# Kernel tuning notes

Hardware: AMD Instinct MI355X
Metric: run time of the kernel (lower is better)

The kernel has to match this reference:

```python
import jax, jax.numpy as jnp
import numpy as np

D_MODEL = 2048
N_HEADS = 16
HEAD_DIM = D_MODEL // N_HEADS
B, T = 4, 2048


def setup_inputs() -> dict:
    key = jax.random.key(0)
    ks = jax.random.split(key, 10)
    s = 1.0 / np.sqrt(D_MODEL)
    x = jax.random.normal(ks[0], (B, T, D_MODEL), dtype=jnp.float32)
    # causal additive mask, broadcastable to [B, H, T, T]
    neg = jnp.finfo(jnp.float32).min
    causal = jnp.triu(jnp.full((T, T), neg, dtype=jnp.float32), k=1)
    mask = causal[None, None, :, :]
    return {
        "x": x,
        "mask": mask,
        "Wq": jax.random.uniform(ks[1], (D_MODEL, D_MODEL), jnp.float32, -s, s),
        "bq": jax.random.uniform(ks[2], (D_MODEL,), jnp.float32, -s, s),
        "Wk": jax.random.uniform(ks[3], (D_MODEL, HEAD_DIM), jnp.float32, -s, s),
        "bk": jax.random.uniform(ks[4], (HEAD_DIM,), jnp.float32, -s, s),
        "Wv": jax.random.uniform(ks[5], (D_MODEL, HEAD_DIM), jnp.float32, -s, s),
        "bv": jax.random.uniform(ks[6], (HEAD_DIM,), jnp.float32, -s, s),
        "Wo": jax.random.uniform(ks[7], (D_MODEL, D_MODEL), jnp.float32, -s, s),
        "bo": jax.random.uniform(ks[8], (D_MODEL,), jnp.float32, -s, s),
    }


def reference(x, mask, Wq, bq, Wk, bk, Wv, bv, Wo, bo):
    Bb, Tt, _ = x.shape
    H, Dh = N_HEADS, HEAD_DIM
    scale = 1.0 / jnp.sqrt(jnp.float32(Dh))
    q = (x @ Wq + bq).reshape(Bb, Tt, H, Dh)          # [B,T,H,D]
    k = x @ Wk + bk                                    # [B,T,D] (single KV head)
    v = x @ Wv + bv                                    # [B,T,D]
    # scores: [B,H,T,T] — q heads against shared k
    attn = jnp.einsum("bthd,bsd->bhts", q, k) * scale
    attn = attn + mask
    attn = jax.nn.softmax(attn, axis=-1)
    out = jnp.einsum("bhts,bsd->bthd", attn, v).reshape(Bb, Tt, D_MODEL)
    return out @ Wo + bo
```

## Files before the change

kernel.cpp:

```cpp
#include <hip/hip_runtime.h>
#include <hip/hip_bf16.h>
#include <stdint.h>

#define DEV __device__ __forceinline__

typedef unsigned short u16;
typedef unsigned int u32;
typedef __bf16 bf16x8 __attribute__((ext_vector_type(8)));
typedef float f32x4 __attribute__((ext_vector_type(4)));
typedef u16 u16x4 __attribute__((ext_vector_type(4)));
typedef u32 u32x4 __attribute__((ext_vector_type(4)));

typedef __attribute__((address_space(1))) u32 u32_as1;
typedef __attribute__((address_space(3))) u32 u32_as3;

static constexpr int Bn = 4, Tn = 2048, Dm = 2048, Hn = 16, Dh = 128;
static constexpr int BT = Bn * Tn;
static constexpr int KVSTR = 256;
static constexpr float CL2 = 0.1275174147f;

#define VMCNT(n) asm volatile("s_waitcnt vmcnt(" #n ")" ::: "memory")
#define BARRIER() __builtin_amdgcn_s_barrier()

DEV u16 f2bf(float f) {
  u32 u = __builtin_bit_cast(u32, f);
  u += 0x7fffu + ((u >> 16) & 1u);
  return (u16)(u >> 16);
}
DEV u16 cvt_bf(float f) { return __builtin_bit_cast(u16, (__bf16)f); }
DEV u32 cvt_pk_bf16(float lo, float hi) {
  u32 r;
  asm("v_cvt_pk_bf16_f32 %0, %1, %2" : "=v"(r) : "v"(lo), "v"(hi));
  return r;
}
DEV float max3f(float a, float b, float c) {
  float d;
  asm("v_max3_f32 %0, %1, %2, %3" : "=v"(d) : "v"(a), "v"(b), "v"(c));
  return d;
}

DEV void gl2lds16(const void* g, void* l) {
  __builtin_amdgcn_global_load_lds((u32_as1*)(uintptr_t)g,
                                   (u32_as3*)(u32)(uintptr_t)l, 16, 0, 0);
}

__global__ __launch_bounds__(256) void k_cast_bf16(const float* __restrict__ in,
                                                   u16* __restrict__ out, int n4) {
  int i = blockIdx.x * 256 + threadIdx.x;
  int stride = gridDim.x * 256;
  for (; i < n4; i += stride) {
    f32x4 v = ((const f32x4*)in)[i];
    u16x4 o;
    o.x = f2bf(v.x); o.y = f2bf(v.y); o.z = f2bf(v.z); o.w = f2bf(v.w);
    ((u16x4*)out)[i] = o;
  }
}

__global__ __launch_bounds__(256) void k_transpose_cast(const float* __restrict__ in,
                                                        u16* __restrict__ out,
                                                        int R, int C) {
  __shared__ float t[32][33];
  const int r0 = blockIdx.y * 32, c0 = blockIdx.x * 32;
  const int x = threadIdx.x, y = threadIdx.y;
#pragma unroll
  for (int i = 0; i < 4; ++i)
    t[y + i * 8][x] = in[(size_t)(r0 + y + i * 8) * C + c0 + x];
  __syncthreads();
#pragma unroll
  for (int i = 0; i < 4; ++i)
    out[(size_t)(c0 + y + i * 8) * R + r0 + x] = f2bf(t[x][y + i * 8]);
}

__global__ __launch_bounds__(256) void k_transpose_v(const u16* __restrict__ in,
                                                     int inStride,
                                                     u16* __restrict__ out,
                                                     int R, int C) {
  __shared__ u16 t[32][34];
  const int r0 = blockIdx.y * 32, c0 = blockIdx.x * 32;
  const int x = threadIdx.x, y = threadIdx.y;
#pragma unroll
  for (int i = 0; i < 4; ++i)
    t[y + i * 8][x] = in[(size_t)(r0 + y + i * 8) * inStride + c0 + x];
  __syncthreads();
  const int sx = (((x & 7) >> 2) << 4) | (((x >> 3) & 3) << 2) | (x & 3);
#pragma unroll
  for (int i = 0; i < 4; ++i)
    out[(size_t)(c0 + y + i * 8) * R + r0 + x] = t[sx][y + i * 8];
}

__global__ void k_concat_bias(const float* __restrict__ a, const float* __restrict__ b,
                              float* __restrict__ dst) {
  int i = threadIdx.x;
  dst[i] = (i < 128) ? a[i] : b[i - 128];
}

template <typename OutT>
__global__ __launch_bounds__(256) void k_gemm_bt(const u16* __restrict__ A,
                                                 const u16* __restrict__ Bt,
                                                 const float* __restrict__ bias,
                                                 OutT* __restrict__ C,
                                                 int M, int N, int K) {
  __shared__ __align__(128) char smem[32768];
  char* As = smem;
  char* Bs = smem + 16384;
  const int tid = threadIdx.x;
  const int wid = tid >> 6, lane = tid & 63;
  const int g = lane >> 4, r = lane & 15;
  const int wr = wid >> 1, wc = wid & 1;
  const int m0 = blockIdx.x * 128, n0 = blockIdx.y * 128;

  f32x4 acc[4][4];
#pragma unroll
  for (int m = 0; m < 4; ++m)
#pragma unroll
    for (int n = 0; n < 4; ++n) acc[m][n] = (f32x4)(0.f);

  for (int k0 = 0; k0 < K; k0 += 64) {
#pragma unroll
    for (int n = 0; n < 4; ++n) {
      const int L = n * 4096 + tid * 16;
      const int row = L >> 7;
      const int colb = (L & 127) ^ ((row & 7) << 4);
      gl2lds16((const char*)A + ((size_t)(m0 + row) * K + k0) * 2 + colb, As + L);
      gl2lds16((const char*)Bt + ((size_t)(n0 + row) * K + k0) * 2 + colb, Bs + L);
    }
    __syncthreads();
#pragma unroll
    for (int kk = 0; kk < 2; ++kk) {
      bf16x8 a[4], b[4];
#pragma unroll
      for (int m = 0; m < 4; ++m) {
        const int row = wr * 64 + m * 16 + r;
        a[m] = *(const bf16x8*)(As + row * 128 + ((kk * 64 + g * 16) ^ ((row & 7) << 4)));
      }
#pragma unroll
      for (int n = 0; n < 4; ++n) {
        const int row = wc * 64 + n * 16 + r;
        b[n] = *(const bf16x8*)(Bs + row * 128 + ((kk * 64 + g * 16) ^ ((row & 7) << 4)));
      }
#pragma unroll
      for (int m = 0; m < 4; ++m)
#pragma unroll
        for (int n = 0; n < 4; ++n)
          acc[m][n] = __builtin_amdgcn_mfma_f32_16x16x32_bf16(a[m], b[n], acc[m][n], 0, 0, 0);
    }
    __syncthreads();
  }

#pragma unroll
  for (int n = 0; n < 4; ++n) {
    const int col = n0 + wc * 64 + n * 16 + r;
    const float bv = bias[col];
#pragma unroll
    for (int m = 0; m < 4; ++m) {
#pragma unroll
      for (int j = 0; j < 4; ++j) {
        const int grow = m0 + wr * 64 + m * 16 + 4 * g + j;
        const float v = acc[m][n][j] + bv;
        if constexpr (sizeof(OutT) == 2)
          ((u16*)C)[(size_t)grow * N + col] = f2bf(v);
        else
          ((float*)C)[(size_t)grow * N + col] = v;
      }
    }
  }
}

template <typename OutT>
__global__ __launch_bounds__(512, 2) void k_gemm256(const u16* __restrict__ A,
                                                    const u16* __restrict__ Bt,
                                                    const float* __restrict__ bias,
                                                    OutT* __restrict__ C,
                                                    int M, int N, int K,
                                                    float oscale) {
  extern __shared__ char smem[];
  const int tid = threadIdx.x;
  const int wid = tid >> 6, lane = tid & 63;
  const int g = lane >> 4, r = lane & 15;
  const int wm = wid >> 2, wn = wid & 3;

  const int nbn = N >> 8;
  const int cpx = gridDim.x >> 3;
  const int linear = (blockIdx.x & 7) * cpx + (blockIdx.x >> 3);
  const int m0 = (linear / nbn) << 8;
  const int n0 = (linear % nbn) << 8;

  const int rowInCh = lane >> 3;
  const int colb = ((lane & 7) << 4) ^ (rowInCh << 4);
  const char* srcA0; const char* srcA1; const char* srcA2; const char* srcA3;
  const char* srcB0; const char* srcB1; const char* srcB2; const char* srcB3;
  int ldsA[4], ldsB[4];
  {
    const int wnh = (wid >> 1) & 1;
    const int cbb = ((wid >> 2) << 1) | (wid & 1);
    const char* sa[4]; const char* sb[4];
#pragma unroll
    for (int i = 0; i < 4; ++i) {
      const int chA = ((wid & 3) << 2) + i;
      const int lrA = (wm << 7) + (chA << 3) + rowInCh;
      sa[i] = (const char*)A + ((size_t)(m0 + lrA) * K) * 2 + colb;
      ldsA[i] = ((wm << 7) + (chA << 3)) * 128 + lane * 16;
      const int chB = (cbb << 2) + i;
      const int lrB = (wnh << 7) + (chB << 3) + rowInCh;
      sb[i] = (const char*)Bt + ((size_t)(n0 + lrB) * K) * 2 + colb;
      ldsB[i] = 32768 + ((wnh << 7) + (chB << 3)) * 128 + lane * 16;
    }
    srcA0 = sa[0]; srcA1 = sa[1]; srcA2 = sa[2]; srcA3 = sa[3];
    srcB0 = sb[0]; srcB1 = sb[1]; srcB2 = sb[2]; srcB3 = sb[3];
  }

  auto stage = [&](int t, int b) {
    const size_t ko = (size_t)t * 128;
    char* base = smem + (b << 16);
    gl2lds16(srcA0 + ko, base + ldsA[0]);
    gl2lds16(srcA1 + ko, base + ldsA[1]);
    gl2lds16(srcA2 + ko, base + ldsA[2]);
    gl2lds16(srcA3 + ko, base + ldsA[3]);
    gl2lds16(srcB0 + ko, base + ldsB[0]);
    gl2lds16(srcB1 + ko, base + ldsB[1]);
    gl2lds16(srcB2 + ko, base + ldsB[2]);
    gl2lds16(srcB3 + ko, base + ldsB[3]);
  };

  f32x4 acc[8][4];
#pragma unroll
  for (int m = 0; m < 8; ++m)
#pragma unroll
    for (int n = 0; n < 4; ++n) acc[m][n] = (f32x4)(0.f);

  auto readA = [&](const char* Ab, int qm, bf16x8 (&a)[8]) {
#pragma unroll
    for (int m = 0; m < 4; ++m) {
      const int row = (wm << 7) + ((qm * 4 + m) << 4) + r;
#pragma unroll
      for (int kk = 0; kk < 2; ++kk)
        a[m * 2 + kk] = *(const bf16x8*)(Ab + row * 128 + ((kk * 64 + g * 16) ^ ((row & 7) << 4)));
    }
  };
  auto readB = [&](const char* Bb, int qn, bf16x8 (&b)[4]) {
#pragma unroll
    for (int n = 0; n < 2; ++n) {
      const int row = (wn << 6) + ((qn * 2 + n) << 4) + r;
#pragma unroll
      for (int kk = 0; kk < 2; ++kk)
        b[n * 2 + kk] = *(const bf16x8*)(Bb + row * 128 + ((kk * 64 + g * 16) ^ ((row & 7) << 4)));
    }
  };
  auto mfmaQ = [&](const bf16x8 (&a)[8], const bf16x8 (&b)[4], int qm, int qn) {
    __builtin_amdgcn_s_setprio(1);
#pragma unroll
    for (int m = 0; m < 4; ++m)
#pragma unroll
      for (int n = 0; n < 2; ++n)
#pragma unroll
        for (int kk = 0; kk < 2; ++kk)
          acc[qm * 4 + m][qn * 2 + n] = __builtin_amdgcn_mfma_f32_16x16x32_bf16(
              a[m * 2 + kk], b[n * 2 + kk], acc[qm * 4 + m][qn * 2 + n], 0, 0, 0);
    __builtin_amdgcn_s_setprio(0);
  };

  const int NT = K >> 6;
  stage(0, 0);
  stage(1, 1);
  VMCNT(8);
  BARRIER();

  bf16x8 a0[8], a1[8], b0[4], b1[4];
  for (int t = 0; t < NT; ++t) {
    const char* Ab = smem + ((t & 1) << 16);
    const char* Bb = Ab + 32768;
    readA(Ab, 0, a0);
    readB(Bb, 0, b0);
    BARRIER();
    mfmaQ(a0, b0, 0, 0);
    BARRIER();
    readB(Bb, 1, b1);
    BARRIER();
    mfmaQ(a0, b1, 0, 1);
    BARRIER();
    readA(Ab, 1, a1);
    BARRIER();
    mfmaQ(a1, b1, 1, 1);
    BARRIER();
    if (t + 2 < NT) {
      stage(t + 2, t & 1);
      mfmaQ(a1, b0, 1, 0);
      VMCNT(8);
    } else {
      mfmaQ(a1, b0, 1, 0);
      VMCNT(0);
    }
    BARRIER();
  }

#pragma unroll
  for (int n = 0; n < 4; ++n) {
    const int col = n0 + wn * 64 + n * 16 + r;
    const float bv = bias[col];
#pragma unroll
    for (int m = 0; m < 8; ++m) {
#pragma unroll
      for (int j = 0; j < 4; ++j) {
        const int grow = m0 + wm * 128 + m * 16 + 4 * g + j;
        const float v = (acc[m][n][j] + bv) * oscale;
        if constexpr (sizeof(OutT) == 2)
          ((u16*)C)[(size_t)grow * N + col] = cvt_bf(v);
        else
          ((float*)C)[(size_t)grow * N + col] = v;
      }
    }
  }
}

__global__ __launch_bounds__(256, 2) void k_attn(const u16* __restrict__ Q,
                                                 const u16* __restrict__ Kb,
                                                 const u16* __restrict__ VT,
                                                 u16* __restrict__ O) {
  __shared__ __align__(1024) char smem[49152];
  char* Vs = smem + 32768;

  const int tid = threadIdx.x;
  const int wq = tid >> 6, lane = tid & 63;
  const int g = lane >> 4, r = lane & 15;

  const int bid = blockIdx.x;
  const int xcd = bid & 7, ii = bid >> 3;
  const int b = xcd >> 1;
  const int h = ((xcd & 1) << 3) | (ii >> 3);
  const int p = ii & 7;
  const int qtA = p, qtB = 15 - p;
  const int nstA = 2 * qtA + 2;
  const int ntot = nstA + 2 * qtB + 2;

  const float DEFER = 8.0f;

  bf16x8 qf[2][4];
  f32x4 o[2][8];
  float mrow[2], lrow[2];

  auto loadQ = [&](int qrow0) {
#pragma unroll
    for (int m2 = 0; m2 < 2; ++m2)
#pragma unroll
      for (int c = 0; c < 4; ++c)
        qf[m2][c] = *(const bf16x8*)(Q + (size_t)(qrow0 + m2 * 16 + r) * Dm + h * Dh + c * 32 + g * 8);
  };
  auto resetAcc = [&]() {
#pragma unroll
    for (int m2 = 0; m2 < 2; ++m2) {
#pragma unroll
      for (int c = 0; c < 8; ++c) o[m2][c] = (f32x4)(0.f);
      mrow[m2] = -1e30f; lrow[m2] = 0.f;
    }
  };
  auto storeO = [&](int qrow0) {
#pragma unroll
    for (int m2 = 0; m2 < 2; ++m2) {
      float linv[4];
#pragma unroll
      for (int j = 0; j < 4; ++j)
        linv[j] = __builtin_amdgcn_rcpf(__shfl(lrow[m2], 20 * g + j));
#pragma unroll
      for (int c = 0; c < 8; ++c)
#pragma unroll
        for (int j = 0; j < 4; ++j)
          O[(size_t)(qrow0 + m2 * 16 + 4 * g + j) * Dm + h * Dh + c * 16 + r] =
              cvt_bf(o[m2][c][j] * linv[j]);
    }
  };
  auto stageK = [&](int s0, char* dst) {
#pragma unroll
    for (int n = 0; n < 4; ++n) {
      const int L = n * 4096 + tid * 16;
      const int row = L >> 8;
      const int colb = (L & 255) ^ ((row & 7) << 4);
      gl2lds16((const char*)Kb + (size_t)(s0 + row) * (KVSTR * 2) + colb, dst + L);
    }
  };
  auto stageV = [&](int s0) {
#pragma unroll
    for (int n = 0; n < 4; ++n) {
      const int L = n * 4096 + tid * 16;
      const int row = L >> 7;
      const int colb = (L & 127) ^ ((row & 7) << 4);
      gl2lds16((const char*)VT + ((size_t)row * BT + s0) * 2 + colb, Vs + L);
    }
  };

  int qt = qtA;
  int qrow0 = b * Tn + qt * 128 + wq * 32;
  int qmin = qt * 128 + wq * 32;
  loadQ(qrow0);
  resetAcc();
  stageK(b * Tn, smem);
  VMCNT(0);
  BARRIER();

  int cur = 0;
  for (int t = 0; t < ntot; ++t) {
    if (t == nstA) {
      storeO(qrow0);
      qt = qtB;
      qrow0 = b * Tn + qt * 128 + wq * 32;
      qmin = qt * 128 + wq * 32;
      loadQ(qrow0);
      resetAcc();
    }
    const int st = (t < nstA) ? t : t - nstA;
    const int s0 = b * Tn + st * 64;

    stageV(s0);
    {
      const int t1 = t + 1;
      const int st1 = (t1 >= ntot) ? 0 : ((t1 < nstA) ? t1 : t1 - nstA);
      stageK(b * Tn + st1 * 64, smem + ((cur ^ 1) << 14));
    }

    const bool fullmask = (st * 64 >= qmin + 32);
    u32x4 pau[2][2];
    if (!fullmask) {
      const char* Kc = smem + (cur << 14);
      f32x4 sf[2][4];
      __builtin_amdgcn_s_setprio(1);
#pragma unroll
      for (int n = 0; n < 4; ++n) {
        f32x4 sa = (f32x4)(0.f), sb = (f32x4)(0.f);
#pragma unroll
        for (int c = 0; c < 4; ++c) {
          const int row = n * 16 + r;
          bf16x8 kf = *(const bf16x8*)(Kc + row * 256 + ((c * 64 + g * 16) ^ ((row & 7) << 4)));
          sa = __builtin_amdgcn_mfma_f32_16x16x32_bf16(kf, qf[0][c], sa, 0, 0, 0);
          sb = __builtin_amdgcn_mfma_f32_16x16x32_bf16(kf, qf[1][c], sb, 0, 0, 0);
        }
        sf[0][n] = sa; sf[1][n] = sb;
      }
      __builtin_amdgcn_s_setprio(0);
      if (st * 64 + 63 > qmin) {
#pragma unroll
        for (int m2 = 0; m2 < 2; ++m2) {
          const int q = qmin + m2 * 16 + r;
#pragma unroll
          for (int n = 0; n < 4; ++n)
#pragma unroll
            for (int j = 0; j < 4; ++j) {
              const int key = st * 64 + n * 16 + 4 * g + j;
              if (key > q) sf[m2][n][j] = -1e30f;
            }
        }
      }
      float vmax[2];
      bool need = false;
#pragma unroll
      for (int m2 = 0; m2 < 2; ++m2) {
        f32x4 t4;
#pragma unroll
        for (int j = 0; j < 4; ++j)
          t4[j] = fmaxf(max3f(sf[m2][0][j], sf[m2][1][j], sf[m2][2][j]), sf[m2][3][j]);
        float v = fmaxf(max3f(t4[0], t4[1], t4[2]), t4[3]);
        v = fmaxf(v, __shfl_xor(v, 16));
        v = fmaxf(v, __shfl_xor(v, 32));
        vmax[m2] = v;
        need = need || (v > mrow[m2] + DEFER);
      }
      if (__any(need)) {
#pragma unroll
        for (int m2 = 0; m2 < 2; ++m2) {
          const float mnew = fmaxf(mrow[m2], vmax[m2]);
          const float fac = __builtin_amdgcn_exp2f(mrow[m2] - mnew);
          mrow[m2] = mnew;
          lrow[m2] *= fac;
#pragma unroll
          for (int j = 0; j < 4; ++j) {
            const float fb = __shfl(fac, 20 * g + j);
#pragma unroll
            for (int c = 0; c < 8; ++c) o[m2][c][j] *= fb;
          }
        }
      }
#pragma unroll
      for (int m2 = 0; m2 < 2; ++m2) {
        float rs = 0.f;
#pragma unroll
        for (int n = 0; n < 4; ++n) {
          const float p0 = __builtin_amdgcn_exp2f(sf[m2][n][0] - mrow[m2]);
          const float p1 = __builtin_amdgcn_exp2f(sf[m2][n][1] - mrow[m2]);
          const float p2 = __builtin_amdgcn_exp2f(sf[m2][n][2] - mrow[m2]);
          const float p3 = __builtin_amdgcn_exp2f(sf[m2][n][3] - mrow[m2]);
          rs += (p0 + p1) + (p2 + p3);
          pau[m2][n >> 1][(n & 1) * 2]     = cvt_pk_bf16(p0, p1);
          pau[m2][n >> 1][(n & 1) * 2 + 1] = cvt_pk_bf16(p2, p3);
        }
        rs += __shfl_xor(rs, 16);
        rs += __shfl_xor(rs, 32);
        lrow[m2] += rs;
      }
    }

    VMCNT(4);
    BARRIER();

    if (!fullmask) {
      __builtin_amdgcn_s_setprio(1);
#pragma unroll
      for (int kk = 0; kk < 2; ++kk) {
        if (st * 64 + kk * 32 >= qmin + 32) continue;
        const bf16x8 pa0 = __builtin_bit_cast(bf16x8, pau[0][kk]);
        const bf16x8 pa1 = __builtin_bit_cast(bf16x8, pau[1][kk]);
#pragma unroll
        for (int c = 0; c < 8; ++c) {
          const int row = c * 16 + r;
          const bf16x8 vb = *(const bf16x8*)(Vs + row * 128 + ((kk * 64 + g * 16) ^ ((row & 7) << 4)));
          o[0][c] = __builtin_amdgcn_mfma_f32_16x16x32_bf16(pa0, vb, o[0][c], 0, 0, 0);
          o[1][c] = __builtin_amdgcn_mfma_f32_16x16x32_bf16(pa1, vb, o[1][c], 0, 0, 0);
        }
      }
      __builtin_amdgcn_s_setprio(0);
    }

    VMCNT(0);
    BARRIER();
    cur ^= 1;
  }
  storeO(qrow0);
}

extern "C" void kernel_launch(void* const* d_in, const int* in_sizes, int n_in,
                              void* d_out, int out_size, void* d_ws, size_t ws_size,
                              hipStream_t stream) {
  const float* x  = (const float*)d_in[0];
  const float* Wq = (const float*)d_in[2];
  const float* bq = (const float*)d_in[3];
  const float* Wk = (const float*)d_in[4];
  const float* bk = (const float*)d_in[5];
  const float* Wv = (const float*)d_in[6];
  const float* bv = (const float*)d_in[7];
  const float* Wo = (const float*)d_in[8];
  const float* bo = (const float*)d_in[9];
  float* out = (float*)d_out;

  char* ws = (char*)d_ws;
  size_t off = 0;
  auto alloc = [&](size_t bytes) {
    char* p = ws + off;
    off += (bytes + 255) & ~(size_t)255;
    return p;
  };
  u16* xb   = (u16*)alloc((size_t)BT * Dm * 2);
  u16* Qb   = (u16*)alloc((size_t)BT * Dm * 2);
  u16* KVb  = (u16*)alloc((size_t)BT * KVSTR * 2);
  u16* VTb  = (u16*)alloc((size_t)BT * Dh * 2);
  u16* Wqt  = (u16*)alloc((size_t)Dm * Dm * 2);
  u16* Wkvt = (u16*)alloc((size_t)Dm * KVSTR * 2);
  u16* Wot  = (u16*)alloc((size_t)Dm * Dm * 2);
  float* bkv = (float*)alloc(KVSTR * sizeof(float));
  u16* Ob   = xb;

  hipFuncSetAttribute(reinterpret_cast<const void*>(&k_gemm256<u16>),
                      hipFuncAttributeMaxDynamicSharedMemorySize, 131072);
  hipFuncSetAttribute(reinterpret_cast<const void*>(&k_gemm256<float>),
                      hipFuncAttributeMaxDynamicSharedMemorySize, 131072);

  k_cast_bf16<<<2048, 256, 0, stream>>>(x, xb, BT * Dm / 4);
  dim3 tb(32, 8);
  k_transpose_cast<<<dim3(Dm / 32, Dm / 32), tb, 0, stream>>>(Wq, Wqt, Dm, Dm);
  k_transpose_cast<<<dim3(Dh / 32, Dm / 32), tb, 0, stream>>>(Wk, Wkvt, Dm, Dh);
  k_transpose_cast<<<dim3(Dh / 32, Dm / 32), tb, 0, stream>>>(Wv, Wkvt + (size_t)Dh * Dm, Dm, Dh);
  k_transpose_cast<<<dim3(Dm / 32, Dm / 32), tb, 0, stream>>>(Wo, Wot, Dm, Dm);
  k_concat_bias<<<1, 256, 0, stream>>>(bk, bv, bkv);

  k_gemm256<u16><<<(BT / 256) * (Dm / 256), 512, 131072, stream>>>(xb, Wqt, bq, Qb, BT, Dm, Dm, CL2);
  k_gemm_bt<u16><<<dim3(BT / 128, KVSTR / 128), 256, 0, stream>>>(xb, Wkvt, bkv, KVb, BT, KVSTR, Dm);
  k_transpose_v<<<dim3(Dh / 32, BT / 32), tb, 0, stream>>>(KVb + Dh, KVSTR, VTb, BT, Dh);

  k_attn<<<512, 256, 0, stream>>>(Qb, KVb, VTb, Ob);

  k_gemm256<float><<<(BT / 256) * (Dm / 256), 512, 131072, stream>>>(Ob, Wot, bo, out, BT, Dm, Dm, 1.0f);
}
```

Measured before the change: 303.7 us.

## Split-K the KV projection and double-buffer V tiles in attention

The KV projection GEMM now runs as a 4-way split-K grid that writes fp32 partials into the Q buffer, followed by a reduce kernel that adds the biases and converts to bf16. This replaces a 128-block launch with 512 blocks to fill more of the GPU and drops the bias concat kernel. The attention kernel now double-buffers V alongside K in 64KB of LDS, prefetching the next tile's V and leaving one wait and barrier per iteration. The cost is extra fp32 partial traffic and a further launch. The larger LDS footprint may also limit attention occupancy.

```diff
diff --git a/kernel.cpp b/kernel.cpp
--- a/kernel.cpp
+++ b/kernel.cpp
@@ -88,17 +88,9 @@
     out[(size_t)(c0 + y + i * 8) * R + r0 + x] = t[sx][y + i * 8];
 }
 
-__global__ void k_concat_bias(const float* __restrict__ a, const float* __restrict__ b,
-                              float* __restrict__ dst) {
-  int i = threadIdx.x;
-  dst[i] = (i < 128) ? a[i] : b[i - 128];
-}
-
-template <typename OutT>
-__global__ __launch_bounds__(256) void k_gemm_bt(const u16* __restrict__ A,
+__global__ __launch_bounds__(256) void k_gemm_kv(const u16* __restrict__ A,
                                                  const u16* __restrict__ Bt,
-                                                 const float* __restrict__ bias,
-                                                 OutT* __restrict__ C,
+                                                 float* __restrict__ P,
                                                  int M, int N, int K) {
   __shared__ __align__(128) char smem[32768];
   char* As = smem;
@@ -108,6 +100,8 @@
   const int g = lane >> 4, r = lane & 15;
   const int wr = wid >> 1, wc = wid & 1;
   const int m0 = blockIdx.x * 128, n0 = blockIdx.y * 128;
+  const int kbase = blockIdx.z * 512;
+  P += (size_t)blockIdx.z * M * N;
 
   f32x4 acc[4][4];
 #pragma unroll
@@ -115,7 +109,7 @@
 #pragma unroll
     for (int n = 0; n < 4; ++n) acc[m][n] = (f32x4)(0.f);
 
-  for (int k0 = 0; k0 < K; k0 += 64) {
+  for (int k0 = kbase; k0 < kbase + 512; k0 += 64) {
 #pragma unroll
     for (int n = 0; n < 4; ++n) {
       const int L = n * 4096 + tid * 16;
@@ -150,20 +144,35 @@
 #pragma unroll
   for (int n = 0; n < 4; ++n) {
     const int col = n0 + wc * 64 + n * 16 + r;
-    const float bv = bias[col];
-#pragma unroll
-    for (int m = 0; m < 4; ++m) {
+#pragma unroll
+    for (int m = 0; m < 4; ++m)
 #pragma unroll
       for (int j = 0; j < 4; ++j) {
         const int grow = m0 + wr * 64 + m * 16 + 4 * g + j;
-        const float v = acc[m][n][j] + bv;
-        if constexpr (sizeof(OutT) == 2)
-          ((u16*)C)[(size_t)grow * N + col] = f2bf(v);
-        else
-          ((float*)C)[(size_t)grow * N + col] = v;
-      }
-    }
-  }
+        P[(size_t)grow * N + col] = acc[m][n][j];
+      }
+  }
+}
+
+__global__ __launch_bounds__(256) void k_kv_reduce(const float* __restrict__ P,
+                                                   const float* __restrict__ bk,
+                                                   const float* __restrict__ bv,
+                                                   u16* __restrict__ KV) {
+  const int i = blockIdx.x * 256 + threadIdx.x;
+  const size_t S = (size_t)BT * KVSTR / 4;
+  f32x4 s0 = ((const f32x4*)P)[i];
+  f32x4 s1 = ((const f32x4*)P)[i + S];
+  f32x4 s2 = ((const f32x4*)P)[i + 2 * S];
+  f32x4 s3 = ((const f32x4*)P)[i + 3 * S];
+  const int col = (i * 4) & (KVSTR - 1);
+  u16x4 o;
+#pragma unroll
+  for (int j = 0; j < 4; ++j) {
+    const int c = col + j;
+    const float b = (c < Dh) ? bk[c] : bv[c - Dh];
+    o[j] = cvt_bf((s0[j] + s1[j]) + (s2[j] + s3[j]) + b);
+  }
+  ((u16x4*)KV)[i] = o;
 }
 
 template <typename OutT>
@@ -316,8 +325,7 @@
                                                  const u16* __restrict__ Kb,
                                                  const u16* __restrict__ VT,
                                                  u16* __restrict__ O) {
-  __shared__ __align__(1024) char smem[49152];
-  char* Vs = smem + 32768;
+  __shared__ __align__(1024) char smem[65536];
 
   const int tid = threadIdx.x;
   const int wq = tid >> 6, lane = tid & 63;
@@ -377,13 +385,13 @@
       gl2lds16((const char*)Kb + (size_t)(s0 + row) * (KVSTR * 2) + colb, dst + L);
     }
   };
-  auto stageV = [&](int s0) {
+  auto stageV = [&](int s0, char* dst) {
 #pragma unroll
     for (int n = 0; n < 4; ++n) {
       const int L = n * 4096 + tid * 16;
       const int row = L >> 7;
       const int colb = (L & 127) ^ ((row & 7) << 4);
-      gl2lds16((const char*)VT + ((size_t)row * BT + s0) * 2 + colb, Vs + L);
+      gl2lds16((const char*)VT + ((size_t)row * BT + s0) * 2 + colb, dst + L);
     }
   };
 
@@ -393,11 +401,13 @@
   loadQ(qrow0);
   resetAcc();
   stageK(b * Tn, smem);
-  VMCNT(0);
-  BARRIER();
+  stageV(b * Tn, smem + 32768);
 
   int cur = 0;
   for (int t = 0; t < ntot; ++t) {
+    VMCNT(0);
+    BARRIER();
+
     if (t == nstA) {
       storeO(qrow0);
       qt = qtB;
@@ -407,19 +417,18 @@
       resetAcc();
     }
     const int st = (t < nstA) ? t : t - nstA;
-    const int s0 = b * Tn + st * 64;
-
-    stageV(s0);
+
     {
       const int t1 = t + 1;
       const int st1 = (t1 >= ntot) ? 0 : ((t1 < nstA) ? t1 : t1 - nstA);
       stageK(b * Tn + st1 * 64, smem + ((cur ^ 1) << 14));
+      stageV(b * Tn + st1 * 64, smem + 32768 + ((cur ^ 1) << 14));
     }
 
     const bool fullmask = (st * 64 >= qmin + 32);
-    u32x4 pau[2][2];
     if (!fullmask) {
       const char* Kc = smem + (cur << 14);
+      const char* Vb = smem + 32768 + (cur << 14);
       f32x4 sf[2][4];
       __builtin_amdgcn_s_setprio(1);
 #pragma unroll
@@ -477,6 +486,7 @@
           }
         }
       }
+      u32x4 pau[2][2];
 #pragma unroll
       for (int m2 = 0; m2 < 2; ++m2) {
         float rs = 0.f;
@@ -494,12 +504,7 @@
         rs += __shfl_xor(rs, 32);
         lrow[m2] += rs;
       }
-    }
-
-    VMCNT(4);
-    BARRIER();
-
-    if (!fullmask) {
+
       __builtin_amdgcn_s_setprio(1);
 #pragma unroll
       for (int kk = 0; kk < 2; ++kk) {
@@ -509,16 +514,13 @@
 #pragma unroll
         for (int c = 0; c < 8; ++c) {
           const int row = c * 16 + r;
-          const bf16x8 vb = *(const bf16x8*)(Vs + row * 128 + ((kk * 64 + g * 16) ^ ((row & 7) << 4)));
+          const bf16x8 vb = *(const bf16x8*)(Vb + row * 128 + ((kk * 64 + g * 16) ^ ((row & 7) << 4)));
           o[0][c] = __builtin_amdgcn_mfma_f32_16x16x32_bf16(pa0, vb, o[0][c], 0, 0, 0);
           o[1][c] = __builtin_amdgcn_mfma_f32_16x16x32_bf16(pa1, vb, o[1][c], 0, 0, 0);
         }
       }
       __builtin_amdgcn_s_setprio(0);
     }
-
-    VMCNT(0);
-    BARRIER();
     cur ^= 1;
   }
   storeO(qrow0);
@@ -552,8 +554,8 @@
   u16* Wqt  = (u16*)alloc((size_t)Dm * Dm * 2);
   u16* Wkvt = (u16*)alloc((size_t)Dm * KVSTR * 2);
   u16* Wot  = (u16*)alloc((size_t)Dm * Dm * 2);
-  float* bkv = (float*)alloc(KVSTR * sizeof(float));
   u16* Ob   = xb;
+  float* Pkv = (float*)Qb;
 
   hipFuncSetAttribute(reinterpret_cast<const void*>(&k_gemm256<u16>),
                       hipFuncAttributeMaxDynamicSharedMemorySize, 131072);
@@ -566,10 +568,11 @@
   k_transpose_cast<<<dim3(Dh / 32, Dm / 32), tb, 0, stream>>>(Wk, Wkvt, Dm, Dh);
   k_transpose_cast<<<dim3(Dh / 32, Dm / 32), tb, 0, stream>>>(Wv, Wkvt + (size_t)Dh * Dm, Dm, Dh);
   k_transpose_cast<<<dim3(Dm / 32, Dm / 32), tb, 0, stream>>>(Wo, Wot, Dm, Dm);
-  k_concat_bias<<<1, 256, 0, stream>>>(bk, bv, bkv);
+
+  k_gemm_kv<<<dim3(BT / 128, KVSTR / 128, 4), 256, 0, stream>>>(xb, Wkvt, Pkv, BT, KVSTR, Dm);
+  k_kv_reduce<<<BT * KVSTR / 4 / 256, 256, 0, stream>>>(Pkv, bk, bv, KVb);
 
   k_gemm256<u16><<<(BT / 256) * (Dm / 256), 512, 131072, stream>>>(xb, Wqt, bq, Qb, BT, Dm, Dm, CL2);
-  k_gemm_bt<u16><<<dim3(BT / 128, KVSTR / 128), 256, 0, stream>>>(xb, Wkvt, bkv, KVb, BT, KVSTR, Dm);
   k_transpose_v<<<dim3(Dh / 32, BT / 32), tb, 0, stream>>>(KVb + Dh, KVSTR, VTb, BT, Dh);
 
   k_attn<<<512, 256, 0, stream>>>(Qb, KVb, VTb, Ob);
```

After: 290.6 us. -4.3%, faster.
